# Performance work log

Measured on AMD Instinct MI355X. Metric: run time of the kernel, lower is better.

Reference implementation:

```python
import jax, jax.numpy as jnp
import numpy as np

N, E = 10000, 320000
IN_CH, HID, OUT_CH, HEADS = 128, 64, 40, 8
NEG_SLOPE = 0.2


def gat_conv(x, src, dst, W, a_src, a_dst, bias, heads, C, concat, n_nodes):
    # x: [N, F_in]; W: [F_in, heads*C]; a_src/a_dst: [heads, C]
    h = (x @ W).reshape(n_nodes, heads, C)              # [N,H,C]
    alpha_src = jnp.sum(h * a_src, axis=-1)             # [N,H]
    alpha_dst = jnp.sum(h * a_dst, axis=-1)             # [N,H]
    score = jax.nn.leaky_relu(alpha_src[src] + alpha_dst[dst], NEG_SLOPE)  # [E,H]
    # segment softmax over edges sharing the same destination node
    smax = jax.ops.segment_max(score, dst, num_segments=n_nodes)
    smax = jnp.where(jnp.isfinite(smax), smax, 0.0)
    ex = jnp.exp(score - smax[dst])
    denom = jax.ops.segment_sum(ex, dst, num_segments=n_nodes)
    alpha = ex / (denom[dst] + 1e-16)                   # [E,H]
    msg = h[src] * alpha[:, :, None]                    # [E,H,C]
    out = jax.ops.segment_sum(msg, dst, num_segments=n_nodes)  # [N,H,C]
    out = out.reshape(n_nodes, heads * C) if concat else out.mean(axis=1)
    return out + bias


def setup_inputs() -> dict:
    key = jax.random.key(0)
    ks = jax.random.split(key, 16)
    g = 0.1
    return {
        "x": jax.random.normal(ks[0], (N, IN_CH), jnp.float32),
        "edge_index": jax.random.randint(ks[1], (2, E), 0, N, jnp.int64),
        "W1": jax.random.normal(ks[2], (IN_CH, HID), jnp.float32) * g,
        "b1": jnp.zeros((HID,), jnp.float32),
        "Wc1": jax.random.normal(ks[3], (HID, HEADS * HID), jnp.float32) * g,
        "att_src1": jax.random.normal(ks[4], (HEADS, HID), jnp.float32) * g,
        "att_dst1": jax.random.normal(ks[5], (HEADS, HID), jnp.float32) * g,
        "bc1": jnp.zeros((HEADS * HID,), jnp.float32),
        "Wc2": jax.random.normal(ks[6], (HEADS * HID, HID), jnp.float32) * g,
        "att_src2": jax.random.normal(ks[7], (1, HID), jnp.float32) * g,
        "att_dst2": jax.random.normal(ks[8], (1, HID), jnp.float32) * g,
        "bc2": jnp.zeros((HID,), jnp.float32),
        "W2": jax.random.normal(ks[9], (HID, OUT_CH), jnp.float32) * g,
        "b2": jnp.zeros((OUT_CH,), jnp.float32),
    }


def reference(x, edge_index, W1, b1, Wc1, att_src1, att_dst1, bc1,
              Wc2, att_src2, att_dst2, bc2, W2, b2):
    # add self-loops (PyG GATConv default add_self_loops=True)
    loop = jnp.arange(N, dtype=edge_index.dtype)
    src = jnp.concatenate([edge_index[0], loop])
    dst = jnp.concatenate([edge_index[1], loop])

    h = jax.nn.relu(x @ W1 + b1)                                   # lin0 + relu (dropout off in eval)
    h = jax.nn.elu(gat_conv(h, src, dst, Wc1, att_src1, att_dst1, bc1,
                            HEADS, HID, True, N))                  # conv1, concat heads
    h = gat_conv(h, src, dst, Wc2, att_src2, att_dst2, bc2,
                 1, HID, False, N)                                 # conv2, single head
    return h @ W2 + b2
```

## Files before the change

kernel.cpp:

```cpp
#include <hip/hip_runtime.h>
#include <cstdint>
#include <cstddef>

#define IN_CH 128
#define HID 64
#define HEADS 8
#define OUT_CH 40
#define NEG 0.2f
#define PAD 128

typedef __attribute__((ext_vector_type(8))) short bf16x8;
typedef __attribute__((ext_vector_type(4))) float f32x4;

#define MFMA(a, b, c) __builtin_amdgcn_mfma_f32_16x16x32_bf16(a, b, c, 0, 0, 0)

__device__ inline unsigned short f2bf(float f) {
    unsigned u = __float_as_uint(f);
    unsigned r = (u + 0x7FFFu + ((u >> 16) & 1u)) >> 16;
    return (unsigned short)r;
}
__device__ inline float bf2f(unsigned short b) {
    return __uint_as_float((unsigned)b << 16);
}
__device__ inline bf16x8 ldb8(const unsigned short* p) {
    return *reinterpret_cast<const bf16x8*>(p);
}


__global__ void k_init(const float* __restrict__ W1,
                       const float* __restrict__ Wc1, const float* __restrict__ Wc2,
                       const float* __restrict__ as1, const float* __restrict__ ad1,
                       int* __restrict__ cursor,
                       unsigned short* __restrict__ W1T,
                       unsigned short* __restrict__ Wc1T, unsigned short* __restrict__ Wc2T,
                       float* __restrict__ va_s, float* __restrict__ va_d, int N) {
    int i = blockIdx.x * 256 + threadIdx.x;
    if (i < N) { cursor[i] = 0; return; }
    i -= N;
    if (i < 64 * 128) {
        int j = i >> 7, k = i & 127;
        W1T[i] = f2bf(W1[k * 64 + j]);
        return;
    }
    i -= 64 * 128;
    if (i < 512 * 64) {
        int j = i >> 6, k = i & 63;
        Wc1T[i] = f2bf(Wc1[(size_t)k * 512 + j]);
        return;
    }
    i -= 512 * 64;
    if (i < 64 * 512) {
        int j = i >> 9, k = i & 511;
        Wc2T[i] = f2bf(Wc2[(size_t)k * 64 + j]);
        return;
    }
    i -= 64 * 512;
    if (i < 1024) {
        int sel = i >> 9, u = i & 511, j = u >> 3, h = u & 7;
        const float* a = sel ? ad1 : as1;
        float sum = 0.f;
        for (int c = 0; c < 64; ++c) sum += Wc1[(size_t)j * 512 + h * 64 + c] * a[h * 64 + c];
        (sel ? va_d : va_s)[j * 8 + h] = sum;
    }
}


__global__ void k_fillpad(const int* __restrict__ ei, int E, int N,
                          int* __restrict__ cursor, int* __restrict__ csrc) {
    int e = blockIdx.x * 256 + threadIdx.x;
    int T = E + N;
    if (e >= T) return;
    int s, d;
    if (e < E) { s = ei[e]; d = ei[E + e]; } else { s = d = e - E; }
    int pos = atomicAdd(&cursor[d], 1);
    csrc[(size_t)d * PAD + pos] = s;
}


__global__ __launch_bounds__(256) void k_lin1m(const float* __restrict__ x,
                                               const unsigned short* __restrict__ W1T,
                                               const float* __restrict__ b1,
                                               const float* __restrict__ va_s, const float* __restrict__ va_d,
                                               unsigned short* __restrict__ h0b,
                                               float* __restrict__ asrc, float* __restrict__ adst, int N) {
    __shared__ float pS[4][16][8], pD[4][16][8];
    int w = threadIdx.x >> 6, l = threadIdx.x & 63;
    int m0 = blockIdx.x * 16;
    int c = l & 15, g = l >> 4;
    bf16x8 af[4];
    const float* arow = x + (size_t)(m0 + c) * 128 + 8 * g;
#pragma unroll
    for (int ks = 0; ks < 4; ++ks) {
        float4 f0 = *(const float4*)(arow + 32 * ks);
        float4 f1 = *(const float4*)(arow + 32 * ks + 4);
        bf16x8 t;
        t[0] = (short)f2bf(f0.x); t[1] = (short)f2bf(f0.y);
        t[2] = (short)f2bf(f0.z); t[3] = (short)f2bf(f0.w);
        t[4] = (short)f2bf(f1.x); t[5] = (short)f2bf(f1.y);
        t[6] = (short)f2bf(f1.z); t[7] = (short)f2bf(f1.w);
        af[ks] = t;
    }
    f32x4 acc = {};
    const unsigned short* brow = W1T + (size_t)(16 * w + c) * 128 + 8 * g;
#pragma unroll
    for (int ks = 0; ks < 4; ++ks) acc = MFMA(af[ks], ldb8(brow + 32 * ks), acc);
    int j = 16 * w + c;
    float bj = b1[j];
    float4 vs0 = *(const float4*)&va_s[j * 8], vs1 = *(const float4*)&va_s[j * 8 + 4];
    float4 vd0 = *(const float4*)&va_d[j * 8], vd1 = *(const float4*)&va_d[j * 8 + 4];
#pragma unroll
    for (int r = 0; r < 4; ++r) {
        float v = fmaxf(acc[r] + bj, 0.f);
        h0b[(size_t)(m0 + 4 * g + r) * 64 + j] = f2bf(v);
        float s0 = v * vs0.x, s1 = v * vs0.y, s2 = v * vs0.z, s3 = v * vs0.w;
        float s4 = v * vs1.x, s5 = v * vs1.y, s6 = v * vs1.z, s7 = v * vs1.w;
        float d0 = v * vd0.x, d1 = v * vd0.y, d2 = v * vd0.z, d3 = v * vd0.w;
        float d4 = v * vd1.x, d5 = v * vd1.y, d6 = v * vd1.z, d7 = v * vd1.w;
#pragma unroll
        for (int off = 1; off < 16; off <<= 1) {
            s0 += __shfl_xor(s0, off); s1 += __shfl_xor(s1, off);
            s2 += __shfl_xor(s2, off); s3 += __shfl_xor(s3, off);
            s4 += __shfl_xor(s4, off); s5 += __shfl_xor(s5, off);
            s6 += __shfl_xor(s6, off); s7 += __shfl_xor(s7, off);
            d0 += __shfl_xor(d0, off); d1 += __shfl_xor(d1, off);
            d2 += __shfl_xor(d2, off); d3 += __shfl_xor(d3, off);
            d4 += __shfl_xor(d4, off); d5 += __shfl_xor(d5, off);
            d6 += __shfl_xor(d6, off); d7 += __shfl_xor(d7, off);
        }
        if (c == 0) {
            int row = 4 * g + r;
            pS[w][row][0] = s0; pS[w][row][1] = s1; pS[w][row][2] = s2; pS[w][row][3] = s3;
            pS[w][row][4] = s4; pS[w][row][5] = s5; pS[w][row][6] = s6; pS[w][row][7] = s7;
            pD[w][row][0] = d0; pD[w][row][1] = d1; pD[w][row][2] = d2; pD[w][row][3] = d3;
            pD[w][row][4] = d4; pD[w][row][5] = d5; pD[w][row][6] = d6; pD[w][row][7] = d7;
        }
    }
    __syncthreads();
    int tid = threadIdx.x;
    if (tid < 128) {
        int row = tid >> 3, h = tid & 7;
        float s = pS[0][row][h] + pS[1][row][h] + pS[2][row][h] + pS[3][row][h];
        float d = pD[0][row][h] + pD[1][row][h] + pD[2][row][h] + pD[3][row][h];
        int n = m0 + row;
        asrc[n * 8 + h] = s;
        adst[n * 8 + h] = d;
    }
}


__global__ __launch_bounds__(128) void k_conv1agg(const unsigned short* __restrict__ h0b,
                                                  const float* __restrict__ asrc, const float* __restrict__ adst,
                                                  const int* __restrict__ degs, const int* __restrict__ csrc,
                                                  unsigned short* __restrict__ aggb, int N) {
    __shared__ int srcb[PAD];
    __shared__ float sb[PAD][8];
    __shared__ float mx[8], den[8], adl[8];
    __shared__ float accsh[512];
    int tid = threadIdx.x;
    int n = blockIdx.x;
    int deg = degs[n];
    if (tid < 8) adl[tid] = adst[n * 8 + tid];
    __syncthreads();
    if (tid < deg) {
        int s = csrc[(size_t)n * PAD + tid];
        srcb[tid] = s;
        const float4* ap = (const float4*)&asrc[(size_t)s * 8];
        float4 a0 = ap[0], a1 = ap[1];
        float v;
        v = a0.x + adl[0]; sb[tid][0] = (v >= 0.f) ? v : NEG * v;
        v = a0.y + adl[1]; sb[tid][1] = (v >= 0.f) ? v : NEG * v;
        v = a0.z + adl[2]; sb[tid][2] = (v >= 0.f) ? v : NEG * v;
        v = a0.w + adl[3]; sb[tid][3] = (v >= 0.f) ? v : NEG * v;
        v = a1.x + adl[4]; sb[tid][4] = (v >= 0.f) ? v : NEG * v;
        v = a1.y + adl[5]; sb[tid][5] = (v >= 0.f) ? v : NEG * v;
        v = a1.z + adl[6]; sb[tid][6] = (v >= 0.f) ? v : NEG * v;
        v = a1.w + adl[7]; sb[tid][7] = (v >= 0.f) ? v : NEG * v;
    }
    __syncthreads();
    if (tid < 64) {
        int hh = tid & 7, idx = tid >> 3;
        float m = -1e30f;
        for (int i = idx; i < deg; i += 8) m = fmaxf(m, sb[i][hh]);
        m = fmaxf(m, __shfl_xor(m, 8));
        m = fmaxf(m, __shfl_xor(m, 16));
        m = fmaxf(m, __shfl_xor(m, 32));
        if (tid < 8) mx[tid] = m;
    }
    __syncthreads();
    for (int idx = tid; idx < deg * 8; idx += 128) {
        int i = idx >> 3, hh = idx & 7;
        sb[i][hh] = __expf(sb[i][hh] - mx[hh]);
    }
    __syncthreads();
    if (tid < 64) {
        int hh = tid & 7, idx = tid >> 3;
        float d = 0.f;
        for (int i = idx; i < deg; i += 8) d += sb[i][hh];
        d += __shfl_xor(d, 8);
        d += __shfl_xor(d, 16);
        d += __shfl_xor(d, 32);
        if (tid < 8) den[tid] = d + 1e-16f;
    }
    int lane = tid & 63, wv = tid >> 6;
    float acc[8] = {0.f, 0.f, 0.f, 0.f, 0.f, 0.f, 0.f, 0.f};
    int i = wv;
    for (; i + 2 < deg; i += 4) {
        float va = bf2f(h0b[(size_t)srcb[i] * 64 + lane]);
        float vb = bf2f(h0b[(size_t)srcb[i + 2] * 64 + lane]);
        float4 wa0 = *(const float4*)&sb[i][0], wa1 = *(const float4*)&sb[i][4];
        float4 wb0 = *(const float4*)&sb[i + 2][0], wb1 = *(const float4*)&sb[i + 2][4];
        acc[0] += wa0.x * va + wb0.x * vb;
        acc[1] += wa0.y * va + wb0.y * vb;
        acc[2] += wa0.z * va + wb0.z * vb;
        acc[3] += wa0.w * va + wb0.w * vb;
        acc[4] += wa1.x * va + wb1.x * vb;
        acc[5] += wa1.y * va + wb1.y * vb;
        acc[6] += wa1.z * va + wb1.z * vb;
        acc[7] += wa1.w * va + wb1.w * vb;
    }
    if (i < deg) {
        float va = bf2f(h0b[(size_t)srcb[i] * 64 + lane]);
        float4 wa0 = *(const float4*)&sb[i][0], wa1 = *(const float4*)&sb[i][4];
        acc[0] += wa0.x * va; acc[1] += wa0.y * va; acc[2] += wa0.z * va; acc[3] += wa0.w * va;
        acc[4] += wa1.x * va; acc[5] += wa1.y * va; acc[6] += wa1.z * va; acc[7] += wa1.w * va;
    }
    __syncthreads();
    if (wv == 1) {
#pragma unroll
        for (int h = 0; h < 8; ++h) accsh[h * 64 + lane] = acc[h];
    }
    __syncthreads();
    if (wv == 0) {
#pragma unroll
        for (int h = 0; h < 8; ++h) {
            float tot = acc[h] + accsh[h * 64 + lane];
            aggb[(size_t)n * 512 + h * 64 + lane] = f2bf(tot / den[h]);
        }
    }
}


__global__ __launch_bounds__(512) void k_post1(const unsigned short* __restrict__ aggb,
                                               const unsigned short* __restrict__ Wc1T,
                                               const float* __restrict__ bc1,
                                               unsigned short* __restrict__ h1b, int N) {
    int h = threadIdx.x >> 6, l = threadIdx.x & 63;
    int m0 = blockIdx.x * 16;
    int c = l & 15, g = l >> 4;
    const unsigned short* arow = aggb + (size_t)(m0 + c) * 512 + h * 64 + 8 * g;
    bf16x8 af0 = ldb8(arow), af1 = ldb8(arow + 32);
    f32x4 acc[4] = {};
#pragma unroll
    for (int nt = 0; nt < 4; ++nt) {
        const unsigned short* brow = Wc1T + (size_t)(h * 64 + 16 * nt + c) * 64 + 8 * g;
        acc[nt] = MFMA(af0, ldb8(brow), acc[nt]);
        acc[nt] = MFMA(af1, ldb8(brow + 32), acc[nt]);
    }
#pragma unroll
    for (int nt = 0; nt < 4; ++nt) {
        int j = h * 64 + 16 * nt + c;
        float bj = bc1[j];
#pragma unroll
        for (int r = 0; r < 4; ++r) {
            float v = acc[nt][r] + bj;
            v = (v > 0.f) ? v : __expf(v) - 1.f;
            h1b[(size_t)(m0 + 4 * g + r) * 512 + j] = f2bf(v);
        }
    }
}


__global__ __launch_bounds__(256) void k_linc2m(const unsigned short* __restrict__ h1b,
                                                const unsigned short* __restrict__ Wc2T,
                                                const float* __restrict__ as2, const float* __restrict__ ad2,
                                                unsigned short* __restrict__ hc2b,
                                                float* __restrict__ asrc, float* __restrict__ adst, int N) {
    __shared__ float part[3][4][64][4];
    int w = threadIdx.x >> 6, l = threadIdx.x & 63;
    int m0 = blockIdx.x * 16;
    int c = l & 15, g = l >> 4;
    const unsigned short* arow = h1b + (size_t)(m0 + c) * 512 + 128 * w + 8 * g;
    f32x4 acc[4] = {};
#pragma unroll
    for (int ks = 0; ks < 4; ++ks) {
        bf16x8 af = ldb8(arow + 32 * ks);
#pragma unroll
        for (int nt = 0; nt < 4; ++nt) {
            const unsigned short* brow = Wc2T + (size_t)(16 * nt + c) * 512 + 128 * w + 32 * ks + 8 * g;
            acc[nt] = MFMA(af, ldb8(brow), acc[nt]);
        }
    }
    if (w > 0) {
#pragma unroll
        for (int nt = 0; nt < 4; ++nt) {
            part[w - 1][nt][l][0] = acc[nt][0];
            part[w - 1][nt][l][1] = acc[nt][1];
            part[w - 1][nt][l][2] = acc[nt][2];
            part[w - 1][nt][l][3] = acc[nt][3];
        }
    }
    __syncthreads();
    if (w != 0) return;
#pragma unroll
    for (int nt = 0; nt < 4; ++nt)
#pragma unroll
        for (int r = 0; r < 4; ++r)
            acc[nt][r] += part[0][nt][l][r] + part[1][nt][l][r] + part[2][nt][l][r];
    float ps[4] = {0.f, 0.f, 0.f, 0.f}, pd[4] = {0.f, 0.f, 0.f, 0.f};
#pragma unroll
    for (int nt = 0; nt < 4; ++nt) {
        int j = 16 * nt + c;
        float aj = as2[j], dj = ad2[j];
#pragma unroll
        for (int r = 0; r < 4; ++r) {
            float v = acc[nt][r];
            hc2b[(size_t)(m0 + 4 * g + r) * 64 + j] = f2bf(v);
            ps[r] += v * aj;
            pd[r] += v * dj;
        }
    }
#pragma unroll
    for (int r = 0; r < 4; ++r) {
        float s = ps[r], d = pd[r];
        s += __shfl_xor(s, 1); s += __shfl_xor(s, 2); s += __shfl_xor(s, 4); s += __shfl_xor(s, 8);
        d += __shfl_xor(d, 1); d += __shfl_xor(d, 2); d += __shfl_xor(d, 4); d += __shfl_xor(d, 8);
        if (c == 0) {
            int n = m0 + 4 * g + r;
            asrc[n] = s;
            adst[n] = d;
        }
    }
}


__global__ __launch_bounds__(256) void k_conv2f(const unsigned short* __restrict__ hc2b,
                                                const float* __restrict__ asrc, const float* __restrict__ adst,
                                                const int* __restrict__ degs, const int* __restrict__ csrc,
                                                const float* __restrict__ bc2,
                                                const float* __restrict__ W2, const float* __restrict__ b2,
                                                float* __restrict__ out, int N) {
    __shared__ float w2s[HID * OUT_CH];
    __shared__ float cosh_[4][HID];
    int tid = threadIdx.x;
    for (int i = tid; i < HID * OUT_CH; i += 256) w2s[i] = W2[i];
    int lane = tid & 63;
    int nl = tid >> 6;
    int n = blockIdx.x * 4 + nl;
    if (n < N) {
        int deg = degs[n];
        float ad = adst[n];
        float rm = -1e30f, rden = 0.f, acc = 0.f;
        for (int base = 0; base < deg; base += 64) {
            int cnt = min(64, deg - base);
            int s = 0;
            float sc = -1e30f;
            if (lane < cnt) {
                s = csrc[(size_t)n * PAD + base + lane];
                float v = asrc[s] + ad;
                sc = (v >= 0.f) ? v : NEG * v;
            }
            float m = sc;
#pragma unroll
            for (int mm = 1; mm < 64; mm <<= 1) m = fmaxf(m, __shfl_xor(m, mm));
            float nmv = fmaxf(rm, m);
            float scale = __expf(rm - nmv);
            float p = (lane < cnt) ? __expf(sc - nmv) : 0.f;
            float d = p;
#pragma unroll
            for (int mm = 1; mm < 64; mm <<= 1) d += __shfl_xor(d, mm);
            rden = rden * scale + d;
            rm = nmv;
            acc *= scale;
            for (int i = 0; i < cnt; ++i) {
                float pi = __shfl(p, i);
                int si = __shfl(s, i);
                acc += pi * bf2f(hc2b[(size_t)si * 64 + lane]);
            }
        }
        cosh_[nl][lane] = acc / (rden + 1e-16f) + bc2[lane];
    }
    __syncthreads();
    if (tid >= 160) return;
    int nn = tid / 40, j = tid % 40;
    int no = blockIdx.x * 4 + nn;
    if (no >= N) return;
    float s = b2[j];
#pragma unroll 8
    for (int k = 0; k < HID; ++k) s += cosh_[nn][k] * w2s[k * OUT_CH + j];
    out[(size_t)no * OUT_CH + j] = s;
}


extern "C" void kernel_launch(void* const* d_in, const int* in_sizes, int n_in,
                              void* d_out, int out_size, void* d_ws, size_t ws_size,
                              hipStream_t stream) {
    const float* x   = (const float*)d_in[0];
    const int*   ei  = (const int*)d_in[1];
    const float* W1  = (const float*)d_in[2];
    const float* b1  = (const float*)d_in[3];
    const float* Wc1 = (const float*)d_in[4];
    const float* as1 = (const float*)d_in[5];
    const float* ad1 = (const float*)d_in[6];
    const float* bc1 = (const float*)d_in[7];
    const float* Wc2 = (const float*)d_in[8];
    const float* as2 = (const float*)d_in[9];
    const float* ad2 = (const float*)d_in[10];
    const float* bc2 = (const float*)d_in[11];
    const float* W2  = (const float*)d_in[12];
    const float* b2  = (const float*)d_in[13];

    const int N = in_sizes[0] / IN_CH;
    const int E = in_sizes[1] / 2;
    const int T = E + N;

    char* base = (char*)d_ws;
    size_t off = 0;
    auto carve = [&](size_t bytes) -> void* {
        off = (off + 255) & ~(size_t)255;
        void* r = base + off;
        off += bytes;
        return r;
    };
    int* cursor     = (int*)carve((size_t)N * 4);
    int* csrc       = (int*)carve((size_t)N * PAD * 4);
    unsigned short* W1T  = (unsigned short*)carve((size_t)64 * 128 * 2);
    unsigned short* Wc1T = (unsigned short*)carve((size_t)512 * 64 * 2);
    unsigned short* Wc2T = (unsigned short*)carve((size_t)64 * 512 * 2);
    float* va_s     = (float*)carve((size_t)512 * 4);
    float* va_d     = (float*)carve((size_t)512 * 4);
    unsigned short* h0b  = (unsigned short*)carve((size_t)N * 64 * 2);
    float* asrc1    = (float*)carve((size_t)N * 8 * 4);
    float* adst1    = (float*)carve((size_t)N * 8 * 4);
    unsigned short* aggb = (unsigned short*)carve((size_t)N * 512 * 2);
    unsigned short* h1b  = (unsigned short*)carve((size_t)N * 512 * 2);
    unsigned short* hc2b = (unsigned short*)carve((size_t)N * 64 * 2);
    float* asrc2    = (float*)carve((size_t)N * 4);
    float* adst2    = (float*)carve((size_t)N * 4);

    int init_total = N + 64 * 128 + 512 * 64 + 64 * 512 + 1024;
    k_init<<<(init_total + 255) / 256, 256, 0, stream>>>(W1, Wc1, Wc2, as1, ad1, cursor,
                                                         W1T, Wc1T, Wc2T, va_s, va_d, N);
    k_fillpad<<<(T + 255) / 256, 256, 0, stream>>>(ei, E, N, cursor, csrc);

    k_lin1m<<<(N + 15) / 16, 256, 0, stream>>>(x, W1T, b1, va_s, va_d, h0b, asrc1, adst1, N);
    k_conv1agg<<<N, 128, 0, stream>>>(h0b, asrc1, adst1, cursor, csrc, aggb, N);
    k_post1<<<(N + 15) / 16, 512, 0, stream>>>(aggb, Wc1T, bc1, h1b, N);

    k_linc2m<<<(N + 15) / 16, 256, 0, stream>>>(h1b, Wc2T, as2, ad2, hc2b, asrc2, adst2, N);
    k_conv2f<<<(N + 3) / 4, 256, 0, stream>>>(hc2b, asrc2, adst2, cursor, csrc, bc2, W2, b2,
                                              (float*)d_out, N);
}
```

Baseline: 118.8 us.

## Fuse post-conv1 projection with conv2 linear, vectorize gathers with paired bf16 loads

Merges the conv1 output projection and ELU kernel with the conv2 linear and attention-logit kernel. The intermediate h1 now stays in shared memory instead of making a round trip through a 10000x512 bf16 global buffer, and one launch is removed. Both gather-aggregation kernels now have each half-wavefront handle a different edge and load two bf16 channels per lane, then combine the halves with a cross-half shuffle. This halves the number of gather iterations but increases register pressure and adds shared-memory use (a larger partial-sum buffer with 8 waves) in the fused kernel.

Result: faster. 109.8 us (-7.6%).

```diff
diff --git a/kernel.cpp b/kernel.cpp
--- a/kernel.cpp
+++ b/kernel.cpp
@@ -202,110 +202,115 @@
         if (tid < 8) den[tid] = d + 1e-16f;
     }
     int lane = tid & 63, wv = tid >> 6;
-    float acc[8] = {0.f, 0.f, 0.f, 0.f, 0.f, 0.f, 0.f, 0.f};
-    int i = wv;
-    for (; i + 2 < deg; i += 4) {
-        float va = bf2f(h0b[(size_t)srcb[i] * 64 + lane]);
-        float vb = bf2f(h0b[(size_t)srcb[i + 2] * 64 + lane]);
-        float4 wa0 = *(const float4*)&sb[i][0], wa1 = *(const float4*)&sb[i][4];
-        float4 wb0 = *(const float4*)&sb[i + 2][0], wb1 = *(const float4*)&sb[i + 2][4];
-        acc[0] += wa0.x * va + wb0.x * vb;
-        acc[1] += wa0.y * va + wb0.y * vb;
-        acc[2] += wa0.z * va + wb0.z * vb;
-        acc[3] += wa0.w * va + wb0.w * vb;
-        acc[4] += wa1.x * va + wb1.x * vb;
-        acc[5] += wa1.y * va + wb1.y * vb;
-        acc[6] += wa1.z * va + wb1.z * vb;
-        acc[7] += wa1.w * va + wb1.w * vb;
-    }
-    if (i < deg) {
-        float va = bf2f(h0b[(size_t)srcb[i] * 64 + lane]);
-        float4 wa0 = *(const float4*)&sb[i][0], wa1 = *(const float4*)&sb[i][4];
-        acc[0] += wa0.x * va; acc[1] += wa0.y * va; acc[2] += wa0.z * va; acc[3] += wa0.w * va;
-        acc[4] += wa1.x * va; acc[5] += wa1.y * va; acc[6] += wa1.z * va; acc[7] += wa1.w * va;
-    }
-    __syncthreads();
-    if (wv == 1) {
-#pragma unroll
-        for (int h = 0; h < 8; ++h) accsh[h * 64 + lane] = acc[h];
-    }
-    __syncthreads();
-    if (wv == 0) {
+    int half = lane >> 5, cl = lane & 31;
+    float accA[8] = {0.f, 0.f, 0.f, 0.f, 0.f, 0.f, 0.f, 0.f};
+    float accB[8] = {0.f, 0.f, 0.f, 0.f, 0.f, 0.f, 0.f, 0.f};
+    for (int i = 2 * wv; i < deg; i += 4) {
+        int e = i + half;
+        float vx = 0.f, vy = 0.f;
+        float4 w0 = {0.f, 0.f, 0.f, 0.f}, w1 = {0.f, 0.f, 0.f, 0.f};
+        if (e < deg) {
+            unsigned u = *(const unsigned*)&h0b[(size_t)srcb[e] * 64 + 2 * cl];
+            vx = bf2f((unsigned short)(u & 0xFFFFu));
+            vy = bf2f((unsigned short)(u >> 16));
+            w0 = *(const float4*)&sb[e][0];
+            w1 = *(const float4*)&sb[e][4];
+        }
+        accA[0] += w0.x * vx; accB[0] += w0.x * vy;
+        accA[1] += w0.y * vx; accB[1] += w0.y * vy;
+        accA[2] += w0.z * vx; accB[2] += w0.z * vy;
+        accA[3] += w0.w * vx; accB[3] += w0.w * vy;
+        accA[4] += w1.x * vx; accB[4] += w1.x * vy;
+        accA[5] += w1.y * vx; accB[5] += w1.y * vy;
+        accA[6] += w1.z * vx; accB[6] += w1.z * vy;
+        accA[7] += w1.w * vx; accB[7] += w1.w * vy;
+    }
+#pragma unroll
+    for (int h = 0; h < 8; ++h) {
+        accA[h] += __shfl_xor(accA[h], 32);
+        accB[h] += __shfl_xor(accB[h], 32);
+    }
+    __syncthreads();
+    if (wv == 1 && half == 0) {
 #pragma unroll
         for (int h = 0; h < 8; ++h) {
-            float tot = acc[h] + accsh[h * 64 + lane];
-            aggb[(size_t)n * 512 + h * 64 + lane] = f2bf(tot / den[h]);
-        }
-    }
-}
-
-
-__global__ __launch_bounds__(512) void k_post1(const unsigned short* __restrict__ aggb,
-                                               const unsigned short* __restrict__ Wc1T,
-                                               const float* __restrict__ bc1,
-                                               unsigned short* __restrict__ h1b, int N) {
-    int h = threadIdx.x >> 6, l = threadIdx.x & 63;
-    int m0 = blockIdx.x * 16;
-    int c = l & 15, g = l >> 4;
-    const unsigned short* arow = aggb + (size_t)(m0 + c) * 512 + h * 64 + 8 * g;
-    bf16x8 af0 = ldb8(arow), af1 = ldb8(arow + 32);
-    f32x4 acc[4] = {};
-#pragma unroll
-    for (int nt = 0; nt < 4; ++nt) {
-        const unsigned short* brow = Wc1T + (size_t)(h * 64 + 16 * nt + c) * 64 + 8 * g;
-        acc[nt] = MFMA(af0, ldb8(brow), acc[nt]);
-        acc[nt] = MFMA(af1, ldb8(brow + 32), acc[nt]);
-    }
-#pragma unroll
-    for (int nt = 0; nt < 4; ++nt) {
-        int j = h * 64 + 16 * nt + c;
-        float bj = bc1[j];
-#pragma unroll
-        for (int r = 0; r < 4; ++r) {
-            float v = acc[nt][r] + bj;
-            v = (v > 0.f) ? v : __expf(v) - 1.f;
-            h1b[(size_t)(m0 + 4 * g + r) * 512 + j] = f2bf(v);
-        }
-    }
-}
-
-
-__global__ __launch_bounds__(256) void k_linc2m(const unsigned short* __restrict__ h1b,
-                                                const unsigned short* __restrict__ Wc2T,
-                                                const float* __restrict__ as2, const float* __restrict__ ad2,
-                                                unsigned short* __restrict__ hc2b,
-                                                float* __restrict__ asrc, float* __restrict__ adst, int N) {
-    __shared__ float part[3][4][64][4];
+            accsh[h * 64 + 2 * cl] = accA[h];
+            accsh[h * 64 + 2 * cl + 1] = accB[h];
+        }
+    }
+    __syncthreads();
+    if (wv == 0 && half == 0) {
+#pragma unroll
+        for (int h = 0; h < 8; ++h) {
+            float t0 = (accA[h] + accsh[h * 64 + 2 * cl]) / den[h];
+            float t1 = (accB[h] + accsh[h * 64 + 2 * cl + 1]) / den[h];
+            unsigned uo = (unsigned)f2bf(t0) | ((unsigned)f2bf(t1) << 16);
+            *(unsigned*)&aggb[(size_t)n * 512 + h * 64 + 2 * cl] = uo;
+        }
+    }
+}
+
+
+__global__ __launch_bounds__(512) void k_p1l2(const unsigned short* __restrict__ aggb,
+                                              const unsigned short* __restrict__ Wc1T,
+                                              const float* __restrict__ bc1,
+                                              const unsigned short* __restrict__ Wc2T,
+                                              const float* __restrict__ as2, const float* __restrict__ ad2,
+                                              unsigned short* __restrict__ hc2b,
+                                              float* __restrict__ asrc, float* __restrict__ adst, int N) {
+    __shared__ unsigned short h1s[16][520];
+    __shared__ float part[7][4][64][4];
     int w = threadIdx.x >> 6, l = threadIdx.x & 63;
     int m0 = blockIdx.x * 16;
     int c = l & 15, g = l >> 4;
-    const unsigned short* arow = h1b + (size_t)(m0 + c) * 512 + 128 * w + 8 * g;
-    f32x4 acc[4] = {};
-#pragma unroll
-    for (int ks = 0; ks < 4; ++ks) {
-        bf16x8 af = ldb8(arow + 32 * ks);
+    {
+        const unsigned short* arow = aggb + (size_t)(m0 + c) * 512 + w * 64 + 8 * g;
+        bf16x8 af0 = ldb8(arow), af1 = ldb8(arow + 32);
+        f32x4 acc[4] = {};
 #pragma unroll
         for (int nt = 0; nt < 4; ++nt) {
-            const unsigned short* brow = Wc2T + (size_t)(16 * nt + c) * 512 + 128 * w + 32 * ks + 8 * g;
-            acc[nt] = MFMA(af, ldb8(brow), acc[nt]);
+            const unsigned short* brow = Wc1T + (size_t)(w * 64 + 16 * nt + c) * 64 + 8 * g;
+            acc[nt] = MFMA(af0, ldb8(brow), acc[nt]);
+            acc[nt] = MFMA(af1, ldb8(brow + 32), acc[nt]);
+        }
+#pragma unroll
+        for (int nt = 0; nt < 4; ++nt) {
+            int j = w * 64 + 16 * nt + c;
+            float bj = bc1[j];
+#pragma unroll
+            for (int r = 0; r < 4; ++r) {
+                float v = acc[nt][r] + bj;
+                v = (v > 0.f) ? v : __expf(v) - 1.f;
+                h1s[4 * g + r][j] = f2bf(v);
+            }
+        }
+    }
+    __syncthreads();
+    f32x4 acc2[4] = {};
+#pragma unroll
+    for (int ks = 0; ks < 2; ++ks) {
+        bf16x8 af = ldb8(&h1s[c][64 * w + 32 * ks + 8 * g]);
+#pragma unroll
+        for (int nt = 0; nt < 4; ++nt) {
+            const unsigned short* brow = Wc2T + (size_t)(16 * nt + c) * 512 + 64 * w + 32 * ks + 8 * g;
+            acc2[nt] = MFMA(af, ldb8(brow), acc2[nt]);
         }
     }
     if (w > 0) {
 #pragma unroll
-        for (int nt = 0; nt < 4; ++nt) {
-            part[w - 1][nt][l][0] = acc[nt][0];
-            part[w - 1][nt][l][1] = acc[nt][1];
-            part[w - 1][nt][l][2] = acc[nt][2];
-            part[w - 1][nt][l][3] = acc[nt][3];
-        }
+        for (int nt = 0; nt < 4; ++nt)
+            *(f32x4*)&part[w - 1][nt][l][0] = acc2[nt];
     }
     __syncthreads();
     if (w != 0) return;
 #pragma unroll
     for (int nt = 0; nt < 4; ++nt)
 #pragma unroll
-        for (int r = 0; r < 4; ++r)
-            acc[nt][r] += part[0][nt][l][r] + part[1][nt][l][r] + part[2][nt][l][r];
+        for (int i = 0; i < 7; ++i) {
+            f32x4 pp = *(const f32x4*)&part[i][nt][l][0];
+            acc2[nt][0] += pp[0]; acc2[nt][1] += pp[1];
+            acc2[nt][2] += pp[2]; acc2[nt][3] += pp[3];
+        }
     float ps[4] = {0.f, 0.f, 0.f, 0.f}, pd[4] = {0.f, 0.f, 0.f, 0.f};
 #pragma unroll
     for (int nt = 0; nt < 4; ++nt) {
@@ -313,7 +318,7 @@
         float aj = as2[j], dj = ad2[j];
 #pragma unroll
         for (int r = 0; r < 4; ++r) {
-            float v = acc[nt][r];
+            float v = acc2[nt][r];
             hc2b[(size_t)(m0 + 4 * g + r) * 64 + j] = f2bf(v);
             ps[r] += v * aj;
             pd[r] += v * dj;
@@ -343,13 +348,14 @@
     __shared__ float cosh_[4][HID];
     int tid = threadIdx.x;
     for (int i = tid; i < HID * OUT_CH; i += 256) w2s[i] = W2[i];
-    int lane = tid & 63;
-    int nl = tid >> 6;
+    int lane = tid & 63, nl = tid >> 6;
+    int half = lane >> 5, cl = lane & 31;
     int n = blockIdx.x * 4 + nl;
     if (n < N) {
         int deg = degs[n];
         float ad = adst[n];
-        float rm = -1e30f, rden = 0.f, acc = 0.f;
+        float rm = -1e30f, rden = 0.f;
+        float ax = 0.f, ay = 0.f;
         for (int base = 0; base < deg; base += 64) {
             int cnt = min(64, deg - base);
             int s = 0;
@@ -370,14 +376,23 @@
             for (int mm = 1; mm < 64; mm <<= 1) d += __shfl_xor(d, mm);
             rden = rden * scale + d;
             rm = nmv;
-            acc *= scale;
-            for (int i = 0; i < cnt; ++i) {
-                float pi = __shfl(p, i);
-                int si = __shfl(s, i);
-                acc += pi * bf2f(hc2b[(size_t)si * 64 + lane]);
+            ax *= scale; ay *= scale;
+            for (int i = 0; i < cnt; i += 2) {
+                int idx = i + half;
+                float pi = __shfl(p, idx);
+                int si = __shfl(s, idx);
+                unsigned u = *(const unsigned*)&hc2b[(size_t)si * 64 + 2 * cl];
+                ax += pi * bf2f((unsigned short)(u & 0xFFFFu));
+                ay += pi * bf2f((unsigned short)(u >> 16));
             }
         }
-        cosh_[nl][lane] = acc / (rden + 1e-16f) + bc2[lane];
+        ax += __shfl_xor(ax, 32);
+        ay += __shfl_xor(ay, 32);
+        if (half == 0) {
+            float inv = 1.f / (rden + 1e-16f);
+            cosh_[nl][2 * cl] = ax * inv + bc2[2 * cl];
+            cosh_[nl][2 * cl + 1] = ay * inv + bc2[2 * cl + 1];
+        }
     }
     __syncthreads();
     if (tid >= 160) return;
@@ -432,7 +447,6 @@
     float* asrc1    = (float*)carve((size_t)N * 8 * 4);
     float* adst1    = (float*)carve((size_t)N * 8 * 4);
     unsigned short* aggb = (unsigned short*)carve((size_t)N * 512 * 2);
-    unsigned short* h1b  = (unsigned short*)carve((size_t)N * 512 * 2);
     unsigned short* hc2b = (unsigned short*)carve((size_t)N * 64 * 2);
     float* asrc2    = (float*)carve((size_t)N * 4);
     float* adst2    = (float*)carve((size_t)N * 4);
@@ -444,9 +458,8 @@
 
     k_lin1m<<<(N + 15) / 16, 256, 0, stream>>>(x, W1T, b1, va_s, va_d, h0b, asrc1, adst1, N);
     k_conv1agg<<<N, 128, 0, stream>>>(h0b, asrc1, adst1, cursor, csrc, aggb, N);
-    k_post1<<<(N + 15) / 16, 512, 0, stream>>>(aggb, Wc1T, bc1, h1b, N);
-
-    k_linc2m<<<(N + 15) / 16, 256, 0, stream>>>(h1b, Wc2T, as2, ad2, hc2b, asrc2, adst2, N);
+    k_p1l2<<<(N + 15) / 16, 512, 0, stream>>>(aggb, Wc1T, bc1, Wc2T, as2, ad2,
+                                              hc2b, asrc2, adst2, N);
     k_conv2f<<<(N + 3) / 4, 256, 0, stream>>>(hc2b, asrc2, adst2, cursor, csrc, bc2, W2, b2,
                                               (float*)d_out, N);
 }
```
